# Kernel optimization log

Measured on AMD Instinct MI355X. Metric: run time of the kernel, lower is better.

The kernel has to match this reference:

```python
import jax, jax.numpy as jnp
import numpy as np

N_NODES = 100000
N_EDGES = 3200000
DIM = 16


def setup_inputs() -> dict:
    key = jax.random.key(0)
    k1, k2, k3, k4 = jax.random.split(key, 4)
    state_input = jax.random.normal(k1, (N_NODES, DIM), dtype=jnp.float32)
    row = jax.random.randint(k2, (N_EDGES,), 0, N_NODES, dtype=jnp.int32)
    col = jax.random.randint(k3, (N_EDGES,), 0, N_NODES, dtype=jnp.int32)
    edge_weights = jax.random.uniform(k4, (N_EDGES,), dtype=jnp.float32)
    return {"state_input": state_input, "row": row, "col": col,
            "edge_weights": edge_weights}


def reference(state_input, row, col, edge_weights):
    # f_eq: per-dim self dynamics, f(x) = -x  -> [N, dim]
    self_diff = -state_input

    # gather pair endpoints: x_1 = state[col], x_2 = state[row]
    # g_eq: sin(x_2 - x_1) per dim (Kuramoto-style coupling) -> [E, dim]
    neighbor_processed = jnp.sin(state_input[row] - state_input[col])

    # weight by edge weight and scatter-sum into destination nodes (col)
    aggregated_sum = jax.ops.segment_sum(
        neighbor_processed * edge_weights[:, None], col,
        num_segments=state_input.shape[0])  # [N, dim]

    # s_eq: elementwise tanh on aggregated sum
    interact_diff = jnp.tanh(aggregated_sum)

    return (self_diff + interact_diff,
            (state_input, self_diff),
            (aggregated_sum, interact_diff))
```

## Files before the change

kernel.cpp:

```cpp
#include <hip/hip_runtime.h>
#include <hip/hip_fp16.h>
#include <math.h>

#define N_NODES 100000
#define N_EDGES 3200000
#define DIM 16
#define NSZ (N_NODES * DIM)

#define NPB 128
#define NBUCK 782
#define NBLK 512
#define EPB 6256
#define MAXCAP 5120
#define CAP 4864
#define PRK 5

typedef float nvec4 __attribute__((ext_vector_type(4)));

__device__ inline unsigned pack32(int c, int r, float ww) {
    unsigned w8 = (unsigned)fminf(ww * 256.0f, 255.0f);
    return ((unsigned)(c & 127) << 25) | ((unsigned)r << 8) | w8;
}

__global__ __launch_bounds__(1024)
void sort_write(const float* __restrict__ state, __half* __restrict__ hs,
                float* __restrict__ out,
                const int* __restrict__ row, const int* __restrict__ col,
                const float* __restrict__ w, int* __restrict__ cnt,
                unsigned* __restrict__ packed) {
    __shared__ int cur[NBUCK];
    int t = threadIdx.x, blk = blockIdx.x;
    int e0 = blk * EPB;
    int eN = e0 + EPB; if (eN > N_EDGES) eN = N_EDGES;
    int nch = (eN - e0) >> 2;
    const int4*   c4p = (const int4*)(col + e0);
    const int4*   r4p = (const int4*)(row + e0);
    const float4* w4p = (const float4*)(w + e0);

    for (int j = t; j < NBUCK; j += 1024) cur[j] = 0;

    {
        int i = blk * 1024 + t;
        if (i < NSZ / 4) {
            nvec4 v = __builtin_nontemporal_load(&((const nvec4*)state)[i]);
            union { __half2 h[2]; float2 f; } u;
            u.h[0] = __floats2half2_rn(v.x, v.y);
            u.h[1] = __floats2half2_rn(v.z, v.w);
            ((float2*)hs)[i] = u.f;
            __builtin_nontemporal_store(v, &((nvec4*)(out + 1 * (size_t)NSZ))[i]);
            nvec4 nv = {-v.x, -v.y, -v.z, -v.w};
            __builtin_nontemporal_store(nv, &((nvec4*)(out + 2 * (size_t)NSZ))[i]);
        }
    }
    __syncthreads();

    unsigned pr[8];
    int bb[8];
    #pragma unroll
    for (int k = 0; k < 2; ++k) {
        int i = t + k * 1024;
        if (i < nch) {
            int4 c = c4p[i]; int4 r = r4p[i]; float4 ww = w4p[i];
            pr[4 * k + 0] = pack32(c.x, r.x, ww.x); bb[4 * k + 0] = c.x >> 7;
            pr[4 * k + 1] = pack32(c.y, r.y, ww.y); bb[4 * k + 1] = c.y >> 7;
            pr[4 * k + 2] = pack32(c.z, r.z, ww.z); bb[4 * k + 2] = c.z >> 7;
            pr[4 * k + 3] = pack32(c.w, r.w, ww.w); bb[4 * k + 3] = c.w >> 7;
            atomicAdd(&cur[bb[4 * k + 0]], 1);
            atomicAdd(&cur[bb[4 * k + 1]], 1);
            atomicAdd(&cur[bb[4 * k + 2]], 1);
            atomicAdd(&cur[bb[4 * k + 3]], 1);
        }
    }
    __syncthreads();

    for (int j = t; j < NBUCK; j += 1024) {
        int v = cur[j];
        if (v) cur[j] = j * MAXCAP + atomicAdd(&cnt[j], v);
    }
    __syncthreads();

    int pos[8];
    #pragma unroll
    for (int k = 0; k < 2; ++k) {
        int i = t + k * 1024;
        if (i < nch) {
            #pragma unroll
            for (int j = 0; j < 4; ++j)
                pos[4 * k + j] = atomicAdd(&cur[bb[4 * k + j]], 1);
        }
    }
    #pragma unroll
    for (int k = 0; k < 2; ++k) {
        int i = t + k * 1024;
        if (i < nch) {
            #pragma unroll
            for (int j = 0; j < 4; ++j)
                packed[pos[4 * k + j]] = pr[4 * k + j];
        }
    }
}

__global__ __launch_bounds__(1024, 8)
void aggregate(const float* __restrict__ state, const __half2* __restrict__ hs2,
               const int* __restrict__ cnt,
               const unsigned* __restrict__ packed,
               float* __restrict__ out) {
    __shared__ unsigned sbuf[CAP];
    __shared__ int s_cnt[NPB], s_start[NPB], s_cur[NPB];
    __shared__ int s_wsum;
    int nb = blockIdx.x, t = threadIdx.x;
    int q = t & 3, sub = (t >> 2) & 1, g = t >> 3;
    int beg = nb * MAXCAP;
    int end = beg + cnt[nb];
    int n = nb * NPB + g;
    bool valid = (n < N_NODES);
    float4 xx = valid ? ((const float4*)state)[n * 4 + q]
                      : make_float4(0.f, 0.f, 0.f, 0.f);
    float4 acc = {0.f, 0.f, 0.f, 0.f};
    const uint2* hsu = (const uint2*)hs2;

    for (int tbeg = beg; tbeg < end; tbeg += CAP) {
        int tend = tbeg + CAP; if (tend > end) tend = end;
        if (t < NPB) s_cnt[t] = 0;
        __syncthreads();

        unsigned pr[PRK];
        #pragma unroll
        for (int k = 0; k < PRK; ++k) {
            int e = tbeg + t + k * 1024;
            if (e < tend) {
                pr[k] = __builtin_nontemporal_load(&packed[e]);
                atomicAdd(&s_cnt[pr[k] >> 25], 1);
            }
        }
        __syncthreads();

        {
            int v = 0, ps = 0;
            if (t < NPB) {
                v = s_cnt[t]; ps = v;
                #pragma unroll
                for (int d = 1; d < 64; d <<= 1) {
                    int u = __shfl_up(ps, d, 64);
                    if ((t & 63) >= d) ps += u;
                }
            }
            if (t == 63) s_wsum = ps;
            __syncthreads();
            if (t < NPB) {
                int ex = ps - v + ((t >= 64) ? s_wsum : 0);
                s_start[t] = ex;
                s_cur[t] = ex;
            }
        }
        __syncthreads();

        int pos[PRK];
        #pragma unroll
        for (int k = 0; k < PRK; ++k) {
            int e = tbeg + t + k * 1024;
            pos[k] = (e < tend) ? atomicAdd(&s_cur[pr[k] >> 25], 1) : -1;
        }
        #pragma unroll
        for (int k = 0; k < PRK; ++k) {
            if (pos[k] >= 0) sbuf[pos[k]] = pr[k];
        }
        __syncthreads();

        {
            int es = s_start[g], ee = s_cur[g];
            int e = es + sub;
            for (; e + 14 < ee; e += 16) {
                unsigned p0 = sbuf[e];
                unsigned p1 = sbuf[e + 2];
                unsigned p2 = sbuf[e + 4];
                unsigned p3 = sbuf[e + 6];
                unsigned p4 = sbuf[e + 8];
                unsigned p5 = sbuf[e + 10];
                unsigned p6 = sbuf[e + 12];
                unsigned p7 = sbuf[e + 14];
                uint2 h0 = hsu[((p0 >> 8) & 0x1FFFFu) * 4u + q];
                uint2 h1 = hsu[((p1 >> 8) & 0x1FFFFu) * 4u + q];
                uint2 h2 = hsu[((p2 >> 8) & 0x1FFFFu) * 4u + q];
                uint2 h3 = hsu[((p3 >> 8) & 0x1FFFFu) * 4u + q];
                uint2 h4 = hsu[((p4 >> 8) & 0x1FFFFu) * 4u + q];
                uint2 h5 = hsu[((p5 >> 8) & 0x1FFFFu) * 4u + q];
                uint2 h6 = hsu[((p6 >> 8) & 0x1FFFFu) * 4u + q];
                uint2 h7 = hsu[((p7 >> 8) & 0x1FFFFu) * 4u + q];
                #pragma unroll
                for (int j = 0; j < 8; ++j) {
                    unsigned p = (j == 0) ? p0 : (j == 1) ? p1 : (j == 2) ? p2
                               : (j == 3) ? p3 : (j == 4) ? p4 : (j == 5) ? p5
                               : (j == 6) ? p6 : p7;
                    uint2 hb = (j == 0) ? h0 : (j == 1) ? h1 : (j == 2) ? h2
                             : (j == 3) ? h3 : (j == 4) ? h4 : (j == 5) ? h5
                             : (j == 6) ? h6 : h7;
                    float we = ((float)(p & 255u) + 0.5f) * 0.00390625f;
                    float2 lo = __half22float2(*(const __half2*)&hb.x);
                    float2 hi = __half22float2(*(const __half2*)&hb.y);
                    acc.x += __sinf(lo.x - xx.x) * we;
                    acc.y += __sinf(lo.y - xx.y) * we;
                    acc.z += __sinf(hi.x - xx.z) * we;
                    acc.w += __sinf(hi.y - xx.w) * we;
                }
            }
            for (; e < ee; e += 2) {
                unsigned p = sbuf[e];
                uint2 hb = hsu[((p >> 8) & 0x1FFFFu) * 4u + q];
                float we = ((float)(p & 255u) + 0.5f) * 0.00390625f;
                float2 lo = __half22float2(*(const __half2*)&hb.x);
                float2 hi = __half22float2(*(const __half2*)&hb.y);
                acc.x += __sinf(lo.x - xx.x) * we;
                acc.y += __sinf(lo.y - xx.y) * we;
                acc.z += __sinf(hi.x - xx.z) * we;
                acc.w += __sinf(hi.y - xx.w) * we;
            }
        }
        __syncthreads();
    }

    acc.x += __shfl_xor(acc.x, 4, 64); acc.y += __shfl_xor(acc.y, 4, 64);
    acc.z += __shfl_xor(acc.z, 4, 64); acc.w += __shfl_xor(acc.w, 4, 64);

    if (valid && sub == 0) {
        float4 th = make_float4(tanhf(acc.x), tanhf(acc.y),
                                tanhf(acc.z), tanhf(acc.w));
        int gdx = n * 4 + q;
        nvec4 v0 = {th.x - xx.x, th.y - xx.y, th.z - xx.z, th.w - xx.w};
        nvec4 v3 = {acc.x, acc.y, acc.z, acc.w};
        nvec4 v4 = {th.x, th.y, th.z, th.w};
        __builtin_nontemporal_store(v0, &((nvec4*)(out + 0 * (size_t)NSZ))[gdx]);
        __builtin_nontemporal_store(v3, &((nvec4*)(out + 3 * (size_t)NSZ))[gdx]);
        __builtin_nontemporal_store(v4, &((nvec4*)(out + 4 * (size_t)NSZ))[gdx]);
    }
}

__global__ __launch_bounds__(256)
void edge_kernel(const float* __restrict__ state, const int* __restrict__ row,
                 const int* __restrict__ col, const float* __restrict__ w,
                 float* __restrict__ agg) {
    int idx = blockIdx.x * blockDim.x + threadIdx.x;
    if (idx >= N_EDGES * 4) return;
    int e = idx >> 2, qq = idx & 3;
    int r = row[e], c = col[e];
    float we = w[e];
    const float4 xr = ((const float4*)state)[r * 4 + qq];
    const float4 xcv = ((const float4*)state)[c * 4 + qq];
    float* dst = agg + c * DIM + qq * 4;
    atomicAdd(dst + 0, sinf(xr.x - xcv.x) * we);
    atomicAdd(dst + 1, sinf(xr.y - xcv.y) * we);
    atomicAdd(dst + 2, sinf(xr.z - xcv.z) * we);
    atomicAdd(dst + 3, sinf(xr.w - xcv.w) * we);
}

__global__ __launch_bounds__(256)
void node_kernel(const float* __restrict__ state, const float* __restrict__ agg,
                 float* __restrict__ out) {
    int idx = blockIdx.x * blockDim.x + threadIdx.x;
    if (idx >= N_NODES * 4) return;
    float4 x = ((const float4*)state)[idx];
    float4 a = ((const float4*)agg)[idx];
    float4 tv = make_float4(tanhf(a.x), tanhf(a.y), tanhf(a.z), tanhf(a.w));
    ((float4*)(out + 0 * NSZ))[idx] = make_float4(tv.x - x.x, tv.y - x.y,
                                                  tv.z - x.z, tv.w - x.w);
    ((float4*)(out + 1 * NSZ))[idx] = x;
    ((float4*)(out + 2 * NSZ))[idx] = make_float4(-x.x, -x.y, -x.z, -x.w);
    ((float4*)(out + 4 * NSZ))[idx] = tv;
}

extern "C" void kernel_launch(void* const* d_in, const int* in_sizes, int n_in,
                              void* d_out, int out_size, void* d_ws, size_t ws_size,
                              hipStream_t stream) {
    const float* state = (const float*)d_in[0];
    const int*   row   = (const int*)d_in[1];
    const int*   col   = (const int*)d_in[2];
    const float* w     = (const float*)d_in[3];
    float* out = (float*)d_out;

    size_t packed_off = 0;
    size_t hs_off     = packed_off + (size_t)NBUCK * MAXCAP * 4;
    size_t cnt_off    = hs_off + (size_t)NSZ * 2;
    size_t needed     = cnt_off + (size_t)NBUCK * 4;

    if (ws_size >= needed) {
        unsigned* packed = (unsigned*)((char*)d_ws + packed_off);
        __half* hs = (__half*)((char*)d_ws + hs_off);
        int* cnt   = (int*)((char*)d_ws + cnt_off);

        (void)hipMemsetAsync(cnt, 0, (size_t)NBUCK * sizeof(int), stream);
        sort_write<<<NBLK, 1024, 0, stream>>>(state, hs, out, row, col, w,
                                              cnt, packed);
        aggregate<<<NBUCK, 1024, 0, stream>>>(
            state, (const __half2*)hs, cnt, packed, out);
    } else {
        float* agg = out + 3 * NSZ;
        (void)hipMemsetAsync(agg, 0, NSZ * sizeof(float), stream);
        edge_kernel<<<(N_EDGES * 4 + 255) / 256, 256, 0, stream>>>(
            state, row, col, w, agg);
        node_kernel<<<(N_NODES * 4 + 255) / 256, 256, 0, stream>>>(
            state, agg, out);
    }
}
```

Before: 148.9 us.

## Replace per-node LDS bucket sort with fixed-point shared-memory atomic accumulation

The aggregate kernel no longer counting-sorts each block's edges by local destination in LDS. Each thread now takes one packed edge, gathers all 16 half-precision source features, and adds fixed-point (scale 2^20) sin terms into a shared int accumulator with LDS atomics. Node state is staged transposed in shared memory. This drops the sort, prefix scan and several barriers, but adds 16 LDS atomics per edge, with contention on high-degree nodes, and brings fixed-point quantization and overflow risk.

```diff
diff --git a/kernel.cpp b/kernel.cpp
--- a/kernel.cpp
+++ b/kernel.cpp
@@ -12,8 +12,6 @@
 #define NBLK 512
 #define EPB 6256
 #define MAXCAP 5120
-#define CAP 4864
-#define PRK 5
 
 typedef float nvec4 __attribute__((ext_vector_type(4)));
 
@@ -105,133 +103,76 @@
                const int* __restrict__ cnt,
                const unsigned* __restrict__ packed,
                float* __restrict__ out) {
-    __shared__ unsigned sbuf[CAP];
-    __shared__ int s_cnt[NPB], s_start[NPB], s_cur[NPB];
-    __shared__ int s_wsum;
+    __shared__ int   s_acc[DIM * NPB];
+    __shared__ float s_xs[DIM * NPB];
     int nb = blockIdx.x, t = threadIdx.x;
-    int q = t & 3, sub = (t >> 2) & 1, g = t >> 3;
+    int n0 = nb * NPB;
+    {
+        int lim = N_NODES - n0; if (lim > NPB) lim = NPB;
+        for (int i = t; i < DIM * NPB; i += 1024) s_acc[i] = 0;
+        for (int i = t; i < NPB * DIM; i += 1024) {
+            int s = i >> 4, d = i & 15;
+            float v = (s < lim) ? state[(size_t)(n0 + s) * DIM + d] : 0.f;
+            s_xs[d * NPB + s] = v;
+        }
+    }
+    __syncthreads();
+
     int beg = nb * MAXCAP;
     int end = beg + cnt[nb];
-    int n = nb * NPB + g;
-    bool valid = (n < N_NODES);
-    float4 xx = valid ? ((const float4*)state)[n * 4 + q]
-                      : make_float4(0.f, 0.f, 0.f, 0.f);
-    float4 acc = {0.f, 0.f, 0.f, 0.f};
     const uint2* hsu = (const uint2*)hs2;
 
-    for (int tbeg = beg; tbeg < end; tbeg += CAP) {
-        int tend = tbeg + CAP; if (tend > end) tend = end;
-        if (t < NPB) s_cnt[t] = 0;
-        __syncthreads();
-
-        unsigned pr[PRK];
+    for (int e = beg + t; e < end; e += 1024) {
+        unsigned p = __builtin_nontemporal_load(&packed[e]);
+        int cl = (int)(p >> 25);
+        unsigned rowid = (p >> 8) & 0x1FFFFu;
+        float ws = ((float)(p & 255u) + 0.5f) * 4096.0f;
+        uint2 h0 = hsu[rowid * 4 + 0];
+        uint2 h1 = hsu[rowid * 4 + 1];
+        uint2 h2 = hsu[rowid * 4 + 2];
+        uint2 h3 = hsu[rowid * 4 + 3];
         #pragma unroll
-        for (int k = 0; k < PRK; ++k) {
-            int e = tbeg + t + k * 1024;
-            if (e < tend) {
-                pr[k] = __builtin_nontemporal_load(&packed[e]);
-                atomicAdd(&s_cnt[pr[k] >> 25], 1);
-            }
-        }
-        __syncthreads();
-
-        {
-            int v = 0, ps = 0;
-            if (t < NPB) {
-                v = s_cnt[t]; ps = v;
-                #pragma unroll
-                for (int d = 1; d < 64; d <<= 1) {
-                    int u = __shfl_up(ps, d, 64);
-                    if ((t & 63) >= d) ps += u;
-                }
-            }
-            if (t == 63) s_wsum = ps;
-            __syncthreads();
-            if (t < NPB) {
-                int ex = ps - v + ((t >= 64) ? s_wsum : 0);
-                s_start[t] = ex;
-                s_cur[t] = ex;
-            }
-        }
-        __syncthreads();
-
-        int pos[PRK];
-        #pragma unroll
-        for (int k = 0; k < PRK; ++k) {
-            int e = tbeg + t + k * 1024;
-            pos[k] = (e < tend) ? atomicAdd(&s_cur[pr[k] >> 25], 1) : -1;
-        }
-        #pragma unroll
-        for (int k = 0; k < PRK; ++k) {
-            if (pos[k] >= 0) sbuf[pos[k]] = pr[k];
-        }
-        __syncthreads();
-
-        {
-            int es = s_start[g], ee = s_cur[g];
-            int e = es + sub;
-            for (; e + 14 < ee; e += 16) {
-                unsigned p0 = sbuf[e];
-                unsigned p1 = sbuf[e + 2];
-                unsigned p2 = sbuf[e + 4];
-                unsigned p3 = sbuf[e + 6];
-                unsigned p4 = sbuf[e + 8];
-                unsigned p5 = sbuf[e + 10];
-                unsigned p6 = sbuf[e + 12];
-                unsigned p7 = sbuf[e + 14];
-                uint2 h0 = hsu[((p0 >> 8) & 0x1FFFFu) * 4u + q];
-                uint2 h1 = hsu[((p1 >> 8) & 0x1FFFFu) * 4u + q];
-                uint2 h2 = hsu[((p2 >> 8) & 0x1FFFFu) * 4u + q];
-                uint2 h3 = hsu[((p3 >> 8) & 0x1FFFFu) * 4u + q];
-                uint2 h4 = hsu[((p4 >> 8) & 0x1FFFFu) * 4u + q];
-                uint2 h5 = hsu[((p5 >> 8) & 0x1FFFFu) * 4u + q];
-                uint2 h6 = hsu[((p6 >> 8) & 0x1FFFFu) * 4u + q];
-                uint2 h7 = hsu[((p7 >> 8) & 0x1FFFFu) * 4u + q];
-                #pragma unroll
-                for (int j = 0; j < 8; ++j) {
-                    unsigned p = (j == 0) ? p0 : (j == 1) ? p1 : (j == 2) ? p2
-                               : (j == 3) ? p3 : (j == 4) ? p4 : (j == 5) ? p5
-                               : (j == 6) ? p6 : p7;
-                    uint2 hb = (j == 0) ? h0 : (j == 1) ? h1 : (j == 2) ? h2
-                             : (j == 3) ? h3 : (j == 4) ? h4 : (j == 5) ? h5
-                             : (j == 6) ? h6 : h7;
-                    float we = ((float)(p & 255u) + 0.5f) * 0.00390625f;
-                    float2 lo = __half22float2(*(const __half2*)&hb.x);
-                    float2 hi = __half22float2(*(const __half2*)&hb.y);
-                    acc.x += __sinf(lo.x - xx.x) * we;
-                    acc.y += __sinf(lo.y - xx.y) * we;
-                    acc.z += __sinf(hi.x - xx.z) * we;
-                    acc.w += __sinf(hi.y - xx.w) * we;
-                }
-            }
-            for (; e < ee; e += 2) {
-                unsigned p = sbuf[e];
-                uint2 hb = hsu[((p >> 8) & 0x1FFFFu) * 4u + q];
-                float we = ((float)(p & 255u) + 0.5f) * 0.00390625f;
-                float2 lo = __half22float2(*(const __half2*)&hb.x);
-                float2 hi = __half22float2(*(const __half2*)&hb.y);
-                acc.x += __sinf(lo.x - xx.x) * we;
-                acc.y += __sinf(lo.y - xx.y) * we;
-                acc.z += __sinf(hi.x - xx.z) * we;
-                acc.w += __sinf(hi.y - xx.w) * we;
-            }
-        }
-        __syncthreads();
-    }
-
-    acc.x += __shfl_xor(acc.x, 4, 64); acc.y += __shfl_xor(acc.y, 4, 64);
-    acc.z += __shfl_xor(acc.z, 4, 64); acc.w += __shfl_xor(acc.w, 4, 64);
-
-    if (valid && sub == 0) {
-        float4 th = make_float4(tanhf(acc.x), tanhf(acc.y),
-                                tanhf(acc.z), tanhf(acc.w));
-        int gdx = n * 4 + q;
-        nvec4 v0 = {th.x - xx.x, th.y - xx.y, th.z - xx.z, th.w - xx.w};
-        nvec4 v3 = {acc.x, acc.y, acc.z, acc.w};
-        nvec4 v4 = {th.x, th.y, th.z, th.w};
-        __builtin_nontemporal_store(v0, &((nvec4*)(out + 0 * (size_t)NSZ))[gdx]);
-        __builtin_nontemporal_store(v3, &((nvec4*)(out + 3 * (size_t)NSZ))[gdx]);
-        __builtin_nontemporal_store(v4, &((nvec4*)(out + 4 * (size_t)NSZ))[gdx]);
+        for (int qq = 0; qq < 4; ++qq) {
+            uint2 hv = (qq == 0) ? h0 : (qq == 1) ? h1 : (qq == 2) ? h2 : h3;
+            float2 lo = __half22float2(*(const __half2*)&hv.x);
+            float2 hi = __half22float2(*(const __half2*)&hv.y);
+            int d = qq * 4;
+            float x0 = s_xs[(d + 0) * NPB + cl];
+            float x1 = s_xs[(d + 1) * NPB + cl];
+            float x2 = s_xs[(d + 2) * NPB + cl];
+            float x3 = s_xs[(d + 3) * NPB + cl];
+            atomicAdd(&s_acc[(d + 0) * NPB + cl], (int)(__sinf(lo.x - x0) * ws));
+            atomicAdd(&s_acc[(d + 1) * NPB + cl], (int)(__sinf(lo.y - x1) * ws));
+            atomicAdd(&s_acc[(d + 2) * NPB + cl], (int)(__sinf(hi.x - x2) * ws));
+            atomicAdd(&s_acc[(d + 3) * NPB + cl], (int)(__sinf(hi.y - x3) * ws));
+        }
+    }
+    __syncthreads();
+
+    if (t < 512) {
+        int s = t >> 2, q = t & 3;
+        int n = n0 + s;
+        if (n < N_NODES) {
+            const float inv = 1.0f / 1048576.0f;
+            int d = q * 4;
+            float4 a = make_float4((float)s_acc[(d + 0) * NPB + s] * inv,
+                                   (float)s_acc[(d + 1) * NPB + s] * inv,
+                                   (float)s_acc[(d + 2) * NPB + s] * inv,
+                                   (float)s_acc[(d + 3) * NPB + s] * inv);
+            float4 xxv = make_float4(s_xs[(d + 0) * NPB + s],
+                                     s_xs[(d + 1) * NPB + s],
+                                     s_xs[(d + 2) * NPB + s],
+                                     s_xs[(d + 3) * NPB + s]);
+            float4 th = make_float4(tanhf(a.x), tanhf(a.y),
+                                    tanhf(a.z), tanhf(a.w));
+            int gdx = n * 4 + q;
+            nvec4 v0 = {th.x - xxv.x, th.y - xxv.y, th.z - xxv.z, th.w - xxv.w};
+            nvec4 v3 = {a.x, a.y, a.z, a.w};
+            nvec4 v4 = {th.x, th.y, th.z, th.w};
+            __builtin_nontemporal_store(v0, &((nvec4*)(out + 0 * (size_t)NSZ))[gdx]);
+            __builtin_nontemporal_store(v3, &((nvec4*)(out + 3 * (size_t)NSZ))[gdx]);
+            __builtin_nontemporal_store(v4, &((nvec4*)(out + 4 * (size_t)NSZ))[gdx]);
+        }
     }
 }
 
```

Result: slower. 154.0 us (+3.4%).
